# Kernel tuning notes

Hardware: AMD Instinct MI355X
Metric: run time of the kernel (lower is better)

The kernel has to match this reference:

```python
import jax, jax.numpy as jnp
import numpy as np

F0 = 39          # FIELD_COUNT
D = 16           # embedding dim
SIZES = [128, 128, 128]  # cross_layer_sizes
B = 8192


def setup_inputs() -> dict:
    key = jax.random.key(0)
    k0, k1, k2, k3, k4 = jax.random.split(key, 5)
    nn_input = jax.random.normal(k0, (B, F0 * D), dtype=jnp.float32)
    # direct=False => field_nums: [39, 64, 64]; filters: [F0*Fk, L]
    scale = 0.02
    f0 = jax.random.normal(k1, (F0 * F0, SIZES[0]), dtype=jnp.float32) * scale
    f1 = jax.random.normal(k2, (F0 * (SIZES[0] // 2), SIZES[1]), dtype=jnp.float32) * scale
    f2 = jax.random.normal(k3, (F0 * (SIZES[1] // 2), SIZES[2]), dtype=jnp.float32) * scale
    final_len = SIZES[0] // 2 + SIZES[1] // 2 + SIZES[2]  # 256
    w_nn = jax.random.normal(k4, (final_len, 1), dtype=jnp.float32) * scale
    b_nn = jnp.zeros((1,), dtype=jnp.float32)
    return {"nn_input": nn_input, "f0": f0, "f1": f1, "f2": f2,
            "w_nn": w_nn, "b_nn": b_nn}


def reference(nn_input, f0, f1, f2, w_nn, b_nn):
    x0 = nn_input.reshape(-1, F0, D)            # [B, F0, D]
    b = x0.shape[0]
    filters = [f0, f1, f2]
    hidden = x0
    field = F0
    direct_outs = []
    n_layers = len(SIZES)
    for idx, layer_size in enumerate(SIZES):
        # dim-wise outer product: z[b,d,i*field+j] = x0[b,i,d]*hidden[b,j,d]
        z = jnp.einsum('bid,bjd->bdij', x0, hidden).reshape(b, D, F0 * field)
        if idx == 0:
            # remove self-interactions: keep strictly upper triangle, x2
            mask = jnp.triu(jnp.ones((F0, F0), dtype=z.dtype), k=1).reshape(1, 1, F0 * F0)
            z = z * mask * 2.0
        # conv1d kernel-width-1 == per-position GEMM; fuse the [0,2,1] transpose
        curr = jnp.einsum('bdc,cl->bld', z, filters[idx])   # [B, L, D]
        curr = jax.nn.relu(curr)                            # cross_activation='relu'
        if idx != n_layers - 1:
            half = layer_size // 2
            next_hidden = curr[:, :half, :]
            direct = curr[:, half:, :]
        else:
            direct = curr
            next_hidden = None
        direct_outs.append(direct)
        hidden = next_hidden
        field = layer_size // 2
    result = jnp.concatenate(direct_outs, axis=1)   # [B, final_len, D]
    rs = result.sum(axis=-1)                        # [B, final_len]
    base_score = rs.sum(axis=1, keepdims=True)      # res=True
    return base_score + rs @ w_nn + b_nn            # [B, 1]
```

## Files before the change

kernel.cpp:

```cpp
#include <hip/hip_runtime.h>


#define F0N 39
#define NC16 156
#define LAYER_HALVES (NC16 * 4 * 64 * 8)

typedef _Float16 half8 __attribute__((ext_vector_type(8)));
typedef float f32x16 __attribute__((ext_vector_type(16)));

__global__ void prep_kernel(const float* __restrict__ f0,
                            const float* __restrict__ f1,
                            const float* __restrict__ f2,
                            _Float16* __restrict__ fprep) {
    int blk  = blockIdx.x;
    int l    = blk / NC16;
    int c16  = blk - l * NC16;
    int t    = threadIdx.x;
    int nt   = t >> 6;
    int lane = t & 63;
    int hf   = lane >> 5;
    int n    = nt * 32 + (lane & 31);
    const float* f = (l == 0) ? f0 : ((l == 1) ? f1 : f2);
    half8 v;
    #pragma unroll
    for (int reg = 0; reg < 8; ++reg) {
        int kg = c16 * 16 + hf * 8 + reg;
        float x;
        if (l == 0) {
            int fi = kg >> 6, fj = kg & 63;
            x = (fj < F0N) ? f[(fi * F0N + fj) * 128 + n] : 0.0f;
        } else {
            x = f[(size_t)kg * 128 + n];
        }
        v[reg] = (_Float16)x;
    }
    *(half8*)&fprep[(size_t)l * LAYER_HALVES + (((c16 * 4 + nt) * 64 + lane) << 3)] = v;
}

#define LOAD_BF(C16)                                                          \
    half8 Bf[4];                                                              \
    {                                                                         \
        _Pragma("unroll")                                                     \
        for (int nt = 0; nt < 4; ++nt)                                        \
            Bf[nt] = *(const half8*)(fpl + ((((C16) * 4 + nt) * 64 + lane) << 3)); \
    }

#define DO_MFMA()                                                             \
    {                                                                         \
        _Pragma("unroll")                                                     \
        for (int mt = 0; mt < 2; ++mt)                                        \
            _Pragma("unroll")                                                 \
            for (int nt = 0; nt < 4; ++nt)                                    \
                acc[mt][nt] = __builtin_amdgcn_mfma_f32_32x32x16_f16(         \
                    Af[mt], Bf[nt], acc[mt][nt], 0, 0, 0);                    \
    }

#define FULL_STEP(Q)                                                          \
    do {                                                                      \
        LOAD_BF(i * 4 + (Q));                                                 \
        half8 Af[2];                                                          \
        _Pragma("unroll")                                                     \
        for (int mt = 0; mt < 2; ++mt) Af[mt] = hreg[mt][(Q)] * xv2[mt];      \
        DO_MFMA();                                                            \
    } while (0)

#define PART_STEP(Q)                                                          \
    do {                                                                      \
        LOAD_BF(i * 4 + (Q));                                                 \
        const int j0 = (Q) * 16 + hf * 8;                                     \
        half8 msk;                                                            \
        _Pragma("unroll")                                                     \
        for (int reg = 0; reg < 8; ++reg)                                     \
            msk[reg] = (j0 + reg > i) ? (_Float16)1.0f : (_Float16)0.0f;      \
        half8 Af[2];                                                          \
        _Pragma("unroll")                                                     \
        for (int mt = 0; mt < 2; ++mt) Af[mt] = hreg[mt][(Q)] * (msk * xv2[mt]); \
        DO_MFMA();                                                            \
    } while (0)

__global__ __launch_bounds__(256, 2) void cin_mfma(
    const float* __restrict__ xin,
    const _Float16* __restrict__ fprep,
    const float* __restrict__ wnn,
    const float* __restrict__ bnn,
    float* __restrict__ out)
{
    __shared__ _Float16 hT[16 * 16 * 72] __attribute__((aligned(16)));
    __shared__ _Float16 xs[16 * 16 * 40] __attribute__((aligned(16)));
    __shared__ float outacc[16];

    const int t     = threadIdx.x;
    const int wave  = t >> 6;
    const int lane  = t & 63;
    const int hf    = lane >> 5;
    const int lane5 = lane & 31;
    const int dl    = lane & 15;
    const int bt    = lane5 >> 4;
    const int wb0   = wave * 4;
    const int b0    = blockIdx.x * 16;

    for (int u = t; u < 2304; u += 256) ((uint4*)hT)[u] = uint4{0, 0, 0, 0};
    if (t < 16) outacc[t] = 0.0f;
    __syncthreads();

    for (int u = t; u < 16 * F0N; u += 256) {
        int nb = u / F0N;
        int i  = u - nb * F0N;
        const float* src = xin + (size_t)(b0 + nb) * 624 + i * 16;
        #pragma unroll
        for (int q = 0; q < 4; ++q) {
            float4 v = *(const float4*)(src + q * 4);
            int d = q * 4;
            hT[(nb * 16 + d + 0) * 72 + i] = (_Float16)v.x;
            hT[(nb * 16 + d + 1) * 72 + i] = (_Float16)v.y;
            hT[(nb * 16 + d + 2) * 72 + i] = (_Float16)v.z;
            hT[(nb * 16 + d + 3) * 72 + i] = (_Float16)v.w;
            xs[(nb * 16 + d + 0) * 40 + i] = (_Float16)v.x;
            xs[(nb * 16 + d + 1) * 40 + i] = (_Float16)v.y;
            xs[(nb * 16 + d + 2) * 40 + i] = (_Float16)v.z;
            xs[(nb * 16 + d + 3) * 40 + i] = (_Float16)v.w;
        }
    }
    __syncthreads();

    for (int layer = 0; layer < 3; ++layer) {
        half8 hreg[2][4];
        #pragma unroll
        for (int mt = 0; mt < 2; ++mt) {
            int base = ((wb0 + mt * 2 + bt) * 16 + dl) * 72 + hf * 8;
            #pragma unroll
            for (int r = 0; r < 4; ++r)
                hreg[mt][r] = *(const half8*)&hT[base + r * 16];
        }
        __syncthreads();

        f32x16 acc[2][4];
        #pragma unroll
        for (int mt = 0; mt < 2; ++mt)
            #pragma unroll
            for (int nt = 0; nt < 4; ++nt)
                #pragma unroll
                for (int e = 0; e < 16; ++e) acc[mt][nt][e] = 0.0f;

        const _Float16* fpl = fprep + (size_t)layer * LAYER_HALVES;
        const int xrow0 = ((wb0 + bt) * 16 + dl) * 40;
        const int xrow1 = ((wb0 + 2 + bt) * 16 + dl) * 40;

        if (layer == 0) {
            _Float16 xv2[2];
            for (int i = 0; i < 16; ++i) {
                xv2[0] = (_Float16)2.0f * xs[xrow0 + i];
                xv2[1] = (_Float16)2.0f * xs[xrow1 + i];
                if (i < 15) PART_STEP(0);
                FULL_STEP(1);
                FULL_STEP(2);
            }
            for (int i = 16; i < 32; ++i) {
                xv2[0] = (_Float16)2.0f * xs[xrow0 + i];
                xv2[1] = (_Float16)2.0f * xs[xrow1 + i];
                if (i < 31) PART_STEP(1);
                FULL_STEP(2);
            }
            for (int i = 32; i < 38; ++i) {
                xv2[0] = (_Float16)2.0f * xs[xrow0 + i];
                xv2[1] = (_Float16)2.0f * xs[xrow1 + i];
                PART_STEP(2);
            }
        } else {
            _Float16 xv2[2];
            for (int i = 0; i < F0N; ++i) {
                xv2[0] = xs[xrow0 + i];
                xv2[1] = xs[xrow1 + i];
                FULL_STEP(0);
                FULL_STEP(1);
                FULL_STEP(2);
                FULL_STEP(3);
            }
        }

        const int catbase = (layer == 2) ? 128 : ((layer == 0) ? -64 : 0);
        #pragma unroll
        for (int mt = 0; mt < 2; ++mt) {
            const int nb0 = wb0 + mt * 2;
            float cm0 = 0.0f, cm1 = 0.0f;
            #pragma unroll
            for (int nt = 0; nt < 4; ++nt) {
                float r[16];
                #pragma unroll
                for (int reg = 0; reg < 16; ++reg)
                    r[reg] = fmaxf(acc[mt][nt][reg], 0.0f);
                if (layer < 2 && nt < 2) {
                    const int j = nt * 32 + lane5;
                    #pragma unroll
                    for (int reg = 0; reg < 16; ++reg) {
                        int nb = nb0 + (reg >> 3);
                        int d  = (reg & 3) + 8 * ((reg >> 2) & 1) + 4 * hf;
                        hT[(nb * 16 + d) * 72 + j] = (_Float16)r[reg];
                    }
                }
                if (layer == 2 || nt >= 2) {
                    const float w = 1.0f + wnn[catbase + nt * 32 + lane5];
                    float s0 = ((r[0] + r[1]) + (r[2] + r[3])) +
                               ((r[4] + r[5]) + (r[6] + r[7]));
                    float s1 = ((r[8] + r[9]) + (r[10] + r[11])) +
                               ((r[12] + r[13]) + (r[14] + r[15]));
                    s0 += __shfl_xor(s0, 32, 64);
                    s1 += __shfl_xor(s1, 32, 64);
                    cm0 = fmaf(s0, w, cm0);
                    cm1 = fmaf(s1, w, cm1);
                }
            }
            #pragma unroll
            for (int sh = 16; sh >= 1; sh >>= 1) {
                cm0 += __shfl_xor(cm0, sh, 64);
                cm1 += __shfl_xor(cm1, sh, 64);
            }
            if (lane == 0) {
                atomicAdd(&outacc[nb0], cm0);
                atomicAdd(&outacc[nb0 + 1], cm1);
            }
        }
        __syncthreads();
    }

    if (t < 16) out[b0 + t] = outacc[t] + bnn[0];
}

extern "C" void kernel_launch(void* const* d_in, const int* in_sizes, int n_in,
                              void* d_out, int out_size, void* d_ws, size_t ws_size,
                              hipStream_t stream) {
    const float* xin = (const float*)d_in[0];
    const float* f0g = (const float*)d_in[1];
    const float* f1g = (const float*)d_in[2];
    const float* f2g = (const float*)d_in[3];
    const float* wnn = (const float*)d_in[4];
    const float* bnn = (const float*)d_in[5];
    float* out = (float*)d_out;
    _Float16* fprep = (_Float16*)d_ws;

    prep_kernel<<<3 * NC16, 256, 0, stream>>>(f0g, f1g, f2g, fprep);

    const int B = in_sizes[0] / 624;
    cin_mfma<<<B / 16, 256, 0, stream>>>(xin, fprep, wnn, bnn, out);
}
```

Before: 253.4 us.

## Split work across 8 waves with one M-tile per wave

Each wave now handles a single 32-row M tile (2 batch elements × 16 dims) instead of two, and the block grows from 4 to 8 waves with launch bounds of 512 threads at 4 blocks per CU. This halves the accumulator and A-fragment registers per wave so more waves can be resident to hide latency. In exchange, every B fragment is loaded from global memory twice as often per block, since each wave reuses it for one M tile instead of two.

```diff
diff --git a/kernel.cpp b/kernel.cpp
--- a/kernel.cpp
+++ b/kernel.cpp
@@ -48,19 +48,15 @@
 #define DO_MFMA()                                                             \
     {                                                                         \
         _Pragma("unroll")                                                     \
-        for (int mt = 0; mt < 2; ++mt)                                        \
-            _Pragma("unroll")                                                 \
-            for (int nt = 0; nt < 4; ++nt)                                    \
-                acc[mt][nt] = __builtin_amdgcn_mfma_f32_32x32x16_f16(         \
-                    Af[mt], Bf[nt], acc[mt][nt], 0, 0, 0);                    \
+        for (int nt = 0; nt < 4; ++nt)                                        \
+            acc[nt] = __builtin_amdgcn_mfma_f32_32x32x16_f16(                 \
+                Afr, Bf[nt], acc[nt], 0, 0, 0);                               \
     }
 
 #define FULL_STEP(Q)                                                          \
     do {                                                                      \
         LOAD_BF(i * 4 + (Q));                                                 \
-        half8 Af[2];                                                          \
-        _Pragma("unroll")                                                     \
-        for (int mt = 0; mt < 2; ++mt) Af[mt] = hreg[mt][(Q)] * xv2[mt];      \
+        half8 Afr = hreg[(Q)] * xv2;                                          \
         DO_MFMA();                                                            \
     } while (0)
 
@@ -72,13 +68,11 @@
         _Pragma("unroll")                                                     \
         for (int reg = 0; reg < 8; ++reg)                                     \
             msk[reg] = (j0 + reg > i) ? (_Float16)1.0f : (_Float16)0.0f;      \
-        half8 Af[2];                                                          \
-        _Pragma("unroll")                                                     \
-        for (int mt = 0; mt < 2; ++mt) Af[mt] = hreg[mt][(Q)] * (msk * xv2[mt]); \
+        half8 Afr = hreg[(Q)] * (msk * xv2);                                  \
         DO_MFMA();                                                            \
     } while (0)
 
-__global__ __launch_bounds__(256, 2) void cin_mfma(
+__global__ __launch_bounds__(512, 4) void cin_mfma(
     const float* __restrict__ xin,
     const _Float16* __restrict__ fprep,
     const float* __restrict__ wnn,
@@ -96,14 +90,14 @@
     const int lane5 = lane & 31;
     const int dl    = lane & 15;
     const int bt    = lane5 >> 4;
-    const int wb0   = wave * 4;
+    const int nb0   = wave * 2;
     const int b0    = blockIdx.x * 16;
 
-    for (int u = t; u < 2304; u += 256) ((uint4*)hT)[u] = uint4{0, 0, 0, 0};
+    for (int u = t; u < 2304; u += 512) ((uint4*)hT)[u] = uint4{0, 0, 0, 0};
     if (t < 16) outacc[t] = 0.0f;
     __syncthreads();
 
-    for (int u = t; u < 16 * F0N; u += 256) {
+    for (int u = t; u < 16 * F0N; u += 512) {
         int nb = u / F0N;
         int i  = u - nb * F0N;
         const float* src = xin + (size_t)(b0 + nb) * 624 + i * 16;
@@ -123,54 +117,46 @@
     }
     __syncthreads();
 
+    const int arow  = (nb0 + bt) * 16 + dl;
+    const int xrow0 = arow * 40;
+
     for (int layer = 0; layer < 3; ++layer) {
-        half8 hreg[2][4];
+        half8 hreg[4];
+        {
+            int base = arow * 72 + hf * 8;
+            #pragma unroll
+            for (int r = 0; r < 4; ++r)
+                hreg[r] = *(const half8*)&hT[base + r * 16];
+        }
+        __syncthreads();
+
+        f32x16 acc[4];
         #pragma unroll
-        for (int mt = 0; mt < 2; ++mt) {
-            int base = ((wb0 + mt * 2 + bt) * 16 + dl) * 72 + hf * 8;
-            #pragma unroll
-            for (int r = 0; r < 4; ++r)
-                hreg[mt][r] = *(const half8*)&hT[base + r * 16];
-        }
-        __syncthreads();
-
-        f32x16 acc[2][4];
-        #pragma unroll
-        for (int mt = 0; mt < 2; ++mt)
-            #pragma unroll
-            for (int nt = 0; nt < 4; ++nt)
-                #pragma unroll
-                for (int e = 0; e < 16; ++e) acc[mt][nt][e] = 0.0f;
+        for (int nt = 0; nt < 4; ++nt)
+            #pragma unroll
+            for (int e = 0; e < 16; ++e) acc[nt][e] = 0.0f;
 
         const _Float16* fpl = fprep + (size_t)layer * LAYER_HALVES;
-        const int xrow0 = ((wb0 + bt) * 16 + dl) * 40;
-        const int xrow1 = ((wb0 + 2 + bt) * 16 + dl) * 40;
 
         if (layer == 0) {
-            _Float16 xv2[2];
             for (int i = 0; i < 16; ++i) {
-                xv2[0] = (_Float16)2.0f * xs[xrow0 + i];
-                xv2[1] = (_Float16)2.0f * xs[xrow1 + i];
+                _Float16 xv2 = (_Float16)2.0f * xs[xrow0 + i];
                 if (i < 15) PART_STEP(0);
                 FULL_STEP(1);
                 FULL_STEP(2);
             }
             for (int i = 16; i < 32; ++i) {
-                xv2[0] = (_Float16)2.0f * xs[xrow0 + i];
-                xv2[1] = (_Float16)2.0f * xs[xrow1 + i];
+                _Float16 xv2 = (_Float16)2.0f * xs[xrow0 + i];
                 if (i < 31) PART_STEP(1);
                 FULL_STEP(2);
             }
             for (int i = 32; i < 38; ++i) {
-                xv2[0] = (_Float16)2.0f * xs[xrow0 + i];
-                xv2[1] = (_Float16)2.0f * xs[xrow1 + i];
+                _Float16 xv2 = (_Float16)2.0f * xs[xrow0 + i];
                 PART_STEP(2);
             }
         } else {
-            _Float16 xv2[2];
             for (int i = 0; i < F0N; ++i) {
-                xv2[0] = xs[xrow0 + i];
-                xv2[1] = xs[xrow1 + i];
+                _Float16 xv2 = xs[xrow0 + i];
                 FULL_STEP(0);
                 FULL_STEP(1);
                 FULL_STEP(2);
@@ -179,16 +165,14 @@
         }
 
         const int catbase = (layer == 2) ? 128 : ((layer == 0) ? -64 : 0);
-        #pragma unroll
-        for (int mt = 0; mt < 2; ++mt) {
-            const int nb0 = wb0 + mt * 2;
+        {
             float cm0 = 0.0f, cm1 = 0.0f;
             #pragma unroll
             for (int nt = 0; nt < 4; ++nt) {
                 float r[16];
                 #pragma unroll
                 for (int reg = 0; reg < 16; ++reg)
-                    r[reg] = fmaxf(acc[mt][nt][reg], 0.0f);
+                    r[reg] = fmaxf(acc[nt][reg], 0.0f);
                 if (layer < 2 && nt < 2) {
                     const int j = nt * 32 + lane5;
                     #pragma unroll
@@ -241,5 +225,5 @@
     prep_kernel<<<3 * NC16, 256, 0, stream>>>(f0g, f1g, f2g, fprep);
 
     const int B = in_sizes[0] / 624;
-    cin_mfma<<<B / 16, 256, 0, stream>>>(xin, fprep, wnn, bnn, out);
+    cin_mfma<<<B / 16, 512, 0, stream>>>(xin, fprep, wnn, bnn, out);
 }
```

Result: slower. 344.5 us (+36.0%).
